# Kernel optimization log

Measured on AMD Instinct MI355X. Metric: run time of the kernel, lower is better.

Reference implementation:

```python
import jax, jax.numpy as jnp
import numpy as np
from jax import lax

B, R, L = 8, 40, 128
IN = 256           # in_size
WDIM = 2 * IN      # word_h feature dim
DREL = 15          # dep_rel_emb_size
F = 200            # num_filters
FH = FW = 3        # filter size
HID = 300          # filter_factory_hidden

leaky = lambda x: jax.nn.leaky_relu(x, 0.01)


def setup_inputs() -> dict:
    key = jax.random.key(0)
    ks = jax.random.split(key, 16)
    s = lambda fan_in: (2.0 / fan_in) ** 0.5  # kaiming-ish scale
    inp = {
        "energy": jax.random.uniform(ks[0], (B, R, L, L), jnp.float32),
        "word_h": jax.random.normal(ks[1], (B, L, WDIM), jnp.float32),
        "e1": jax.random.normal(ks[2], (B, WDIM), jnp.float32),
        "e2": jax.random.normal(ks[3], (B, WDIM), jnp.float32),
        "sent_len": jax.random.randint(ks[4], (B,), 1, L, jnp.int64 if jax.config.jax_enable_x64 else jnp.int32),
        # params
        "rel_embs": jax.random.normal(ks[5], (R, DREL), jnp.float32) * s(DREL),
        "arc_W": jax.random.normal(ks[6], (IN, 4 * IN + DREL), jnp.float32) * s(4 * IN + DREL),
        "arc_b": jnp.zeros((IN,), jnp.float32),
        "ff_W": jax.random.normal(ks[7], (HID, 4 * IN), jnp.float32) * s(4 * IN),
        "ff_b": jnp.zeros((HID,), jnp.float32),
        "fw1": jax.random.normal(ks[8], (F, IN, FH, FW, HID), jnp.float32) * s(HID),
        "fb1": jax.random.normal(ks[9], (F, IN, FH, FW), jnp.float32) * 0.02,
        "it_W": jax.random.normal(ks[10], (F, 4 * IN), jnp.float32) * s(4 * IN),
        "it_b": jnp.zeros((F,), jnp.float32),
    }
    return inp


def _forward(energy, word_h, e1, e2, rel_embs, arc_W, arc_b, ff_W, ff_b, fw1, fb1, it_W, it_b):
    # threshold mask (energy_threshold = 0.0)
    energy = jnp.where(energy < 0.0, 0.0, energy)

    # ---- get_arc_representations ----
    marginal = energy.sum(axis=1)                                  # [B,L,L]
    rel_tensor = jnp.einsum('brij,rd->bijd', energy, rel_embs)     # [B,L,L,DREL]
    # combine_two_tensors(word_h, word_h): Z[b,i,j] = [X[b,j], Y[b,i]]
    X2 = jnp.broadcast_to(word_h[:, None, :, :], (B, L, L, WDIM))
    Y2 = jnp.broadcast_to(word_h[:, :, None, :], (B, L, L, WDIM))
    dep_head = jnp.concatenate([X2, Y2], axis=-1) * marginal[..., None]  # [B,L,L,4*IN]
    all_t = jnp.concatenate([dep_head, rel_tensor], axis=-1)       # [B,L,L,4*IN+DREL]
    arc = leaky(jnp.einsum('bijk,ok->bijo', all_t, arc_W) + arc_b) # [B,L,L,IN]
    mem_bank = jnp.transpose(arc, (0, 3, 1, 2))                    # [B,IN,L,L]

    # ---- filter factory (dropout = identity at eval) ----
    inputs = jnp.concatenate([e1, e2], axis=-1)                    # [B,4*IN]
    h = leaky(inputs @ ff_W.T + ff_b)                              # [B,HID]
    filt = leaky(jnp.einsum('fdhwk,bk->bfdhw', fw1, h) + fb1)      # [B,F,IN,3,3]

    # ---- per-sample conv2d, batched via vmap ----
    def conv_one(x, w):  # x: [IN,L,L], w: [F,IN,3,3]
        return lax.conv_general_dilated(x[None], w, (1, 1), 'VALID',
                                        dimension_numbers=('NCHW', 'OIHW', 'NCHW'))[0]
    out = jax.vmap(conv_one)(mem_bank, filt)                       # [B,F,L-2,L-2]
    result = leaky(out).reshape(B, F, -1).max(axis=-1)             # adaptive max pool -> [B,F]

    transformed = leaky(inputs @ it_W.T + it_b)                    # [B,F]
    return transformed + result


def reference(energy, word_h, e1, e2, sent_len, rel_embs, arc_W, arc_b,
              ff_W, ff_b, fw1, fb1, it_W, it_b):
    del sent_len  # unused by the original forward path
    return _forward(energy, word_h, e1, e2, rel_embs, arc_W, arc_b,
                    ff_W, ff_b, fw1, fb1, it_W, it_b)
```

## Files before the change

kernel.cpp:

```cpp
#include <hip/hip_runtime.h>
#include <stdint.h>


#define LK(x) ((x) > 0.f ? (x) : 0.01f*(x))

typedef __attribute__((ext_vector_type(8))) short s16x8;
typedef __attribute__((ext_vector_type(4))) float f32x4;

__device__ __forceinline__ unsigned short f2bf(float f) {
  union { float f; unsigned int u; } v; v.f = f;
  unsigned int u = v.u;
  return (unsigned short)((u + 0x7FFFu + ((u >> 16) & 1u)) >> 16);
}

__device__ __forceinline__ void gload_lds16(const void* g, void* l) {
  __builtin_amdgcn_global_load_lds(
      (const __attribute__((address_space(1))) unsigned int*)g,
      (__attribute__((address_space(3))) unsigned int*)l, 16, 0, 0);
}

__global__ __launch_bounds__(256) void k_prep(
    const float* __restrict__ e1, const float* __restrict__ e2,
    const float* __restrict__ rel, const float* __restrict__ aW,
    const float* __restrict__ ffW, const float* __restrict__ ffb,
    const float* __restrict__ itW, const float* __restrict__ itb,
    const float* __restrict__ wh,
    unsigned short* __restrict__ whbf, unsigned short* __restrict__ aw1,
    unsigned short* __restrict__ aw2, unsigned short* __restrict__ rwt,
    float* __restrict__ hg, float* __restrict__ trans)
{
  int bid = blockIdx.x, t = threadIdx.x;
  if (bid < 16) {
    __shared__ float in_lds[1024];
    int b = bid & 7;
    for (int k = t; k < 1024; k += 256)
      in_lds[k] = (k < 512) ? e1[b*512 + k] : e2[b*512 + (k - 512)];
    __syncthreads();
    if (bid < 8) {
      for (int o = t; o < 300; o += 256) {
        const float4* wr = (const float4*)(ffW + (size_t)o*1024);
        float acc = ffb[o];
        for (int k = 0; k < 256; ++k) {
          float4 w = wr[k]; float4 v = *(const float4*)&in_lds[k*4];
          acc += w.x*v.x + w.y*v.y + w.z*v.z + w.w*v.w;
        }
        hg[b*300 + o] = LK(acc);
      }
    } else {
      for (int o = t; o < 200; o += 256) {
        const float4* wr = (const float4*)(itW + (size_t)o*1024);
        float acc = itb[o];
        for (int k = 0; k < 256; ++k) {
          float4 w = wr[k]; float4 v = *(const float4*)&in_lds[k*4];
          acc += w.x*v.x + w.y*v.y + w.z*v.z + w.w*v.w;
        }
        trans[b*200 + o] = LK(acc);
      }
    }
  } else if (bid < 80) {
    int id0 = (bid - 16)*256 + t;
    for (int v = id0; v < 131072; v += 64*256) {
      float4 x = ((const float4*)wh)[v];
      unsigned short* dst = whbf + (size_t)v*4;
      dst[0] = f2bf(x.x); dst[1] = f2bf(x.y); dst[2] = f2bf(x.z); dst[3] = f2bf(x.w);
    }
  } else if (bid < 144) {
    int id0 = (bid - 80)*256 + t;
    for (int e = id0; e < 131072; e += 64*256) {
      int o = e >> 9, k = e & 511;
      aw1[e] = f2bf(aW[(size_t)o*1039 + k]);
      aw2[e] = f2bf(aW[(size_t)o*1039 + 512 + k]);
    }
  } else {
    int o = t;
    for (int r = 0; r < 40; ++r) {
      float s = 0.f;
      for (int d = 0; d < 15; ++d) s += rel[r*15 + d] * aW[(size_t)o*1039 + 1024 + d];
      rwt[o*72 + r] = f2bf(s);
    }
    for (int r = 40; r < 72; ++r) rwt[o*72 + r] = 0;
  }
}

__global__ __launch_bounds__(256) void k_pq(
    const unsigned short* __restrict__ whbf,
    const unsigned short* __restrict__ aw1,
    const unsigned short* __restrict__ aw2,
    float* __restrict__ Pg, float* __restrict__ Qg)
{
  int bid = blockIdx.x, t = threadIdx.x;
  int g = bid >> 8;
  int wv = t >> 6, l = t & 63, lm = l & 15, hi = l >> 4;
  int tile = (bid & 255)*4 + wv;
  int ot = tile & 15, nt = tile >> 4;
  const unsigned short* A = g ? aw2 : aw1;
  float* out = g ? Qg : Pg;
  int orow = ot*16 + lm, n = nt*16 + lm;
  f32x4 acc = {0.f, 0.f, 0.f, 0.f};
  const unsigned short* ap = A + (size_t)orow*512 + hi*8;
  const unsigned short* bp = whbf + (size_t)n*512 + hi*8;
#pragma unroll
  for (int kk = 0; kk < 16; ++kk) {
    s16x8 af = *(const s16x8*)(ap + kk*32);
    s16x8 bf = *(const s16x8*)(bp + kk*32);
    acc = __builtin_amdgcn_mfma_f32_16x16x32_bf16(bf, af, acc, 0, 0, 0);
  }
  int nb = nt*16 + hi*4, o = ot*16 + lm;
#pragma unroll
  for (int r = 0; r < 4; ++r)
    out[(size_t)(nb + r)*256 + o] = acc[r];
}

__global__ __launch_bounds__(256) void k_filt(
    const float* __restrict__ fw1, const float* __restrict__ fb1,
    const float* __restrict__ hg, unsigned short* __restrict__ filtX)
{
  int bid = blockIdx.x, t = threadIdx.x;
  __shared__ __align__(16) unsigned short Abuf[64*320];
  __shared__ __align__(16) unsigned short Bbuf[16*320];
  int r0 = bid*64;
  for (int idx = t; idx < 640; idx += 256) {
    int n = idx / 40, kc = idx - (idx/40)*40;
    unsigned w[4];
#pragma unroll
    for (int j = 0; j < 8; j += 2) {
      int k = kc*8 + j;
      float a = (n < 8 && k   < 300) ? hg[n*300 + k]     : 0.f;
      float b = (n < 8 && k+1 < 300) ? hg[n*300 + k + 1] : 0.f;
      w[j>>1] = (unsigned)f2bf(a) | ((unsigned)f2bf(b) << 16);
    }
    int byte = (n*640 + kc*16) ^ ((n & 7) << 4);
    *(uint4*)((char*)Bbuf + byte) = *(uint4*)w;
  }
  const float4* src = (const float4*)(fw1 + (size_t)r0*300);
  for (int i = 0; i < 19; ++i) {
    int c4 = t + i*256;
    if (c4 < 4800) {
      float4 v = src[c4];
      int row = c4 / 75, k = (c4 - row*75)*4;
      unsigned lo  = (unsigned)f2bf(v.x) | ((unsigned)f2bf(v.y) << 16);
      unsigned hi2 = (unsigned)f2bf(v.z) | ((unsigned)f2bf(v.w) << 16);
      int byte = (row*640 + k*2) ^ ((row & 7) << 4);
      *(unsigned long long*)((char*)Abuf + byte) =
          (unsigned long long)lo | ((unsigned long long)hi2 << 32);
    }
  }
  for (int idx = t; idx < 320; idx += 256) {
    int row = idx / 5, c = idx - (idx/5)*5;
    int byte = (row*640 + 600 + c*8) ^ ((row & 7) << 4);
    *(unsigned long long*)((char*)Abuf + byte) = 0ULL;
  }
  __syncthreads();
  int wv = t >> 6, l = t & 63, lm = l & 15, hi = l >> 4;
  int arow = wv*16 + lm;
  f32x4 acc = {0.f, 0.f, 0.f, 0.f};
#pragma unroll
  for (int ks = 0; ks < 10; ++ks) {
    int abyte = (arow*640 + ks*64 + hi*16) ^ ((arow & 7) << 4);
    int bbyte = (lm*640   + ks*64 + hi*16) ^ ((lm   & 7) << 4);
    s16x8 af = *(const s16x8*)((char*)Abuf + abyte);
    s16x8 bf = *(const s16x8*)((char*)Bbuf + bbyte);
    acc = __builtin_amdgcn_mfma_f32_16x16x32_bf16(af, bf, acc, 0, 0, 0);
  }
  if (lm < 8) {
#pragma unroll
    for (int r = 0; r < 4; ++r) {
      int wrow = r0 + wv*16 + hi*4 + r;
      float v = LK(acc[r] + fb1[wrow]);
      filtX[(size_t)wrow*8 + lm] = f2bf(v);
    }
  }
}

__global__ __launch_bounds__(256) void k_tr(
    const unsigned short* __restrict__ filtX,
    unsigned short* __restrict__ filtg)
{
  __shared__ unsigned short sh[8*2312];
  int bid = blockIdx.x, t = threadIdx.x;
  int dc = bid >> 5, fch = bid & 31;
  if (fch >= 25) {
    uint4 z = {0,0,0,0};
#pragma unroll
    for (int i = 0; i < 9; ++i) {
      int idx = t + i*256;
      int b = idx / 288, rem = idx - b*288;
      char* dst = (char*)filtg + ((size_t)(b*8+dc)*256 + fch*8)*576 + rem*16;
      *(uint4*)dst = z;
    }
    return;
  }
#pragma unroll
  for (int i = 0; i < 9; ++i) {
    int rr = t + i*256;
    int f_loc = rr / 288, e = rr - f_loc*288;
    int dl = e / 9, tap = e - dl*9;
    size_t wrow = (size_t)(fch*8 + f_loc)*2304 + dc*288 + e;
    uint4 v = *(const uint4*)((const char*)filtX + wrow*16);
    const unsigned short* pv = (const unsigned short*)&v;
    int base = f_loc*288 + tap*32 + dl;
#pragma unroll
    for (int b = 0; b < 8; ++b)
      sh[b*2312 + base] = pv[b];
  }
  __syncthreads();
#pragma unroll
  for (int i = 0; i < 9; ++i) {
    int idx = t + i*256;
    int b = idx / 288, rem = idx - b*288;
    uint4 v = *(const uint4*)((const char*)sh + b*4624 + rem*16);
    char* dst = (char*)filtg + ((size_t)(b*8+dc)*256 + fch*8)*576 + rem*16;
    *(uint4*)dst = v;
  }
}

__global__ __launch_bounds__(256) void k_arc(
    const float* __restrict__ energy,
    const unsigned short* __restrict__ rwt,
    const float* __restrict__ Pg, const float* __restrict__ Qg,
    const float* __restrict__ arcb,
    unsigned short* __restrict__ memb)
{
  __shared__ unsigned short Et[128*72];
  __shared__ float mpart[256];
  __shared__ float qlds[256];
  __shared__ float blds[256];
  int bid = blockIdx.x, t = threadIdx.x;
  int b = bid >> 7, i = bid & 127;
  int jj = t & 127, half = t >> 7;
  float macc = 0.f;
  for (int rr = 0; rr < 20; ++rr) {
    int r = half*20 + rr;
    float e = energy[(((size_t)b*40 + r)*128 + i)*128 + jj];
    e = fmaxf(e, 0.f);
    macc += e;
    Et[jj*72 + r] = f2bf(e);
  }
  mpart[t] = macc;
  if (t < 128) {
#pragma unroll
    for (int r = 40; r < 72; ++r) Et[t*72 + r] = 0;
  }
  qlds[t] = Qg[((size_t)(b*128 + i))*256 + t];
  blds[t] = arcb[t];
  __syncthreads();

  int wv = t >> 6, l = t & 63, lm = l & 15, hi = l >> 4;
  unsigned short* mout = memb + ((size_t)(b*128 + i))*128*256;
  for (int otl = 0; otl < 4; ++otl) {
    int ocb = (wv*4 + otl)*16;
    const unsigned short* rp = rwt + (ocb + lm)*72 + hi*8;
    s16x8 rw0 = *(const s16x8*)rp;
    s16x8 rw1 = *(const s16x8*)(rp + 32);
    int oc0 = ocb + hi*4;
    float4 q4 = *(const float4*)&qlds[oc0];
    float4 b4 = *(const float4*)&blds[oc0];
    for (int jt = 0; jt < 8; ++jt) {
      const unsigned short* ep = &Et[(jt*16 + lm)*72 + hi*8];
      s16x8 et0 = *(const s16x8*)ep;
      s16x8 et1 = *(const s16x8*)(ep + 32);
      f32x4 acc = {0.f,0.f,0.f,0.f};
      acc = __builtin_amdgcn_mfma_f32_16x16x32_bf16(rw0, et0, acc, 0, 0, 0);
      acc = __builtin_amdgcn_mfma_f32_16x16x32_bf16(rw1, et1, acc, 0, 0, 0);
      int j = jt*16 + lm;
      float m = mpart[j] + mpart[128 + j];
      float4 p4 = *(const float4*)&Pg[((size_t)(b*128 + j))*256 + oc0];
      unsigned long long pk = 0;
#pragma unroll
      for (int r = 0; r < 4; ++r) {
        float pr = (r==0)?p4.x:((r==1)?p4.y:((r==2)?p4.z:p4.w));
        float qr = (r==0)?q4.x:((r==1)?q4.y:((r==2)?q4.z:q4.w));
        float br = (r==0)?b4.x:((r==1)?b4.y:((r==2)?b4.z:b4.w));
        float v = acc[r] + m*(pr + qr) + br;
        v = LK(v);
        pk |= ((unsigned long long)f2bf(v)) << (16*r);
      }
      *(unsigned long long*)(mout + (size_t)j*256 + oc0) = pk;
    }
  }
}

__global__ __launch_bounds__(256, 2) void k_conv(
    const unsigned short* __restrict__ filtg,
    const unsigned short* __restrict__ memb,
    float* __restrict__ part)
{
  __shared__ __align__(16) char smem[50688];
  int t = threadIdx.x;
  int bid = (blockIdx.x & 7)*128 + (blockIdx.x >> 3);
  int yq = bid & 31;
  int tmp = bid >> 5;
  int fc = tmp & 3, b = tmp >> 2;
  int y0 = yq*4;
  int wv = t >> 6, l = t & 63, lm = l & 15, hi = l >> 4;
  int wx = wv & 1, wf = wv >> 1;

  f32x4 zero = {0.f,0.f,0.f,0.f};
  f32x4 acc[4][4][2];
#pragma unroll
  for (int yb = 0; yb < 4; ++yb)
#pragma unroll
    for (int xt = 0; xt < 4; ++xt) { acc[yb][xt][0] = zero; acc[yb][xt][1] = zero; }

  const char* fb0 = (const char*)filtg +
      ((size_t)(b*8)*256 + fc*64 + wf*32 + lm)*576 + hi*16;

  for (int dc = 0; dc < 8; ++dc) {
    s16x8 freg[2][9];
    const char* fdc = fb0 + (size_t)dc*(256*576);
#pragma unroll
    for (int ft = 0; ft < 2; ++ft)
#pragma unroll
      for (int tap = 0; tap < 9; ++tap)
        freg[ft][tap] = *(const s16x8*)(fdc + ft*(16*576) + tap*64);
    for (int c = wv; c < 50; c += 4) {
      int id = c*64 + l;
      if (id < 3168) {
        int ky = id / 528;
        int rem = id - ky*528;
        int x = rem >> 2, s = rem & 3;
        int cs = s ^ ((x >> 1) & 3);
        int xs = (x < 128) ? x : 127;
        int row = y0 + ky; if (row > 127) row = 127;
        const char* ms = (const char*)memb +
            (((((size_t)(b*128 + row))*128 + xs)*256) + dc*32 + cs*8)*2;
        gload_lds16(ms, smem + c*1024);
      }
    }
    __syncthreads();
#pragma unroll
    for (int r = 0; r < 6; ++r) {
#pragma unroll
      for (int kx = 0; kx < 3; ++kx) {
#pragma unroll
        for (int xt = 0; xt < 4; ++xt) {
          int x = wx*64 + xt*16 + lm + kx;
          int slot = hi ^ ((x >> 1) & 3);
          s16x8 af = *(const s16x8*)(smem + ((r*132 + x)*4 + slot)*16);
#pragma unroll
          for (int yb = 0; yb < 4; ++yb) {
            const int ky = r - yb;
            if (ky >= 0 && ky <= 2) {
              acc[yb][xt][0] = __builtin_amdgcn_mfma_f32_16x16x32_bf16(af, freg[0][ky*3+kx], acc[yb][xt][0], 0,0,0);
              acc[yb][xt][1] = __builtin_amdgcn_mfma_f32_16x16x32_bf16(af, freg[1][ky*3+kx], acc[yb][xt][1], 0,0,0);
            }
          }
        }
      }
    }
    __syncthreads();
  }

  float pm[4][2];
#pragma unroll
  for (int yb = 0; yb < 4; ++yb) { pm[yb][0] = -3.4e38f; pm[yb][1] = -3.4e38f; }
#pragma unroll
  for (int yb = 0; yb < 4; ++yb)
#pragma unroll
    for (int xt = 0; xt < 4; ++xt) {
      int xb = wx*64 + xt*16 + hi*4;
#pragma unroll
      for (int r = 0; r < 4; ++r) {
        if (xb + r < 126) {
          pm[yb][0] = fmaxf(pm[yb][0], acc[yb][xt][0][r]);
          pm[yb][1] = fmaxf(pm[yb][1], acc[yb][xt][1][r]);
        }
      }
    }
#pragma unroll
  for (int yb = 0; yb < 4; ++yb)
#pragma unroll
    for (int ft = 0; ft < 2; ++ft) {
      pm[yb][ft] = fmaxf(pm[yb][ft], __shfl_xor(pm[yb][ft], 16));
      pm[yb][ft] = fmaxf(pm[yb][ft], __shfl_xor(pm[yb][ft], 32));
    }
  float* red = (float*)smem;
  if (l < 16) {
#pragma unroll
    for (int yb = 0; yb < 4; ++yb)
#pragma unroll
      for (int ft = 0; ft < 2; ++ft)
        red[(yb*4 + wf*2 + wx)*32 + ft*16 + lm] = pm[yb][ft];
  }
  __syncthreads();
  {
    int yb = t >> 6, tt = t & 63;
    int wfi = tt >> 5, fi = tt & 31;
    if (y0 + yb < 126) {
      float v = fmaxf(red[(yb*4 + wfi*2 + 0)*32 + fi], red[(yb*4 + wfi*2 + 1)*32 + fi]);
      v = LK(v);
      part[((size_t)(b*126 + y0 + yb))*256 + fc*64 + tt] = v;
    }
  }
}

__global__ __launch_bounds__(256) void k_final(
    const float* __restrict__ part, const float* __restrict__ trans,
    float* __restrict__ out)
{
  int bid = blockIdx.x, t = threadIdx.x;
  int b = bid >> 3, fg = bid & 7;
  int f = fg*32 + (t >> 3), ys = t & 7;
  float m = -3.4e38f;
  for (int yy = ys; yy < 126; yy += 8)
    m = fmaxf(m, part[((size_t)(b*126 + yy))*256 + f]);
  m = fmaxf(m, __shfl_xor(m, 1));
  m = fmaxf(m, __shfl_xor(m, 2));
  m = fmaxf(m, __shfl_xor(m, 4));
  if (ys == 0 && f < 200)
    out[b*200 + f] = trans[b*200 + f] + m;
}

extern "C" void kernel_launch(void* const* d_in, const int* in_sizes, int n_in,
                              void* d_out, int out_size, void* d_ws, size_t ws_size,
                              hipStream_t stream)
{
  (void)in_sizes; (void)n_in; (void)out_size; (void)ws_size;
  const float* energy = (const float*)d_in[0];
  const float* word_h = (const float*)d_in[1];
  const float* e1     = (const float*)d_in[2];
  const float* e2     = (const float*)d_in[3];
  const float* rel    = (const float*)d_in[5];
  const float* aW     = (const float*)d_in[6];
  const float* arcb   = (const float*)d_in[7];
  const float* ffW    = (const float*)d_in[8];
  const float* ffb    = (const float*)d_in[9];
  const float* fw1    = (const float*)d_in[10];
  const float* fb1    = (const float*)d_in[11];
  const float* itW    = (const float*)d_in[12];
  const float* itb    = (const float*)d_in[13];

  char* ws = (char*)d_ws;
  unsigned short* whbf  = (unsigned short*)(ws + 0);
  unsigned short* aw1   = (unsigned short*)(ws + 1048576);
  unsigned short* aw2   = (unsigned short*)(ws + 1310720);
  unsigned short* rwt   = (unsigned short*)(ws + 1572864);
  float*          hg    = (float*)(ws + 1609728);
  float*          trans = (float*)(ws + 1619328);
  float*          Pg    = (float*)(ws + 1625728);
  float*          Qg    = (float*)(ws + 2674304);
  float*          part  = (float*)(ws + 3722880);
  unsigned short* filtg = (unsigned short*)(ws + 4755072);
  unsigned short* memb  = (unsigned short*)(ws + 14454400);
  unsigned short* filtX = (unsigned short*)(ws + 81563264);

  k_prep <<<145, 256, 0, stream>>>(e1, e2, rel, aW, ffW, ffb, itW, itb, word_h,
                                   whbf, aw1, aw2, rwt, hg, trans);
  k_pq   <<<512, 256, 0, stream>>>(whbf, aw1, aw2, Pg, Qg);
  k_filt <<<7200, 256, 0, stream>>>(fw1, fb1, hg, filtX);
  k_tr   <<<256, 256, 0, stream>>>(filtX, filtg);
  k_arc  <<<1024, 256, 0, stream>>>(energy, rwt, Pg, Qg, arcb, memb);
  k_conv <<<1024, 256, 0, stream>>>(filtg, memb, part);
  k_final<<<64, 256, 0, stream>>>(part, trans, (float*)d_out);
}
```

Measured before the change: 366.3 us.

## Parallelize prep GEMVs across waves and stream fw1 directly into MFMA registers

The small e1/e2 matvecs in k_prep previously ran on 16 blocks with one thread per output looping over 1024 inputs. They now run on 1000 blocks, each wave computing one output with a 64-lane shuffle reduction. In k_filt the fw1 tile is no longer staged through swizzled LDS: each lane loads its fp32 row slice from global memory, converts it to bf16 in registers and feeds it straight to the MFMA. This drops a large LDS buffer and a staging pass, at the cost of less coalesced global reads in k_filt.

```diff
diff --git a/kernel.cpp b/kernel.cpp
--- a/kernel.cpp
+++ b/kernel.cpp
@@ -30,42 +30,40 @@
     float* __restrict__ hg, float* __restrict__ trans)
 {
   int bid = blockIdx.x, t = threadIdx.x;
-  if (bid < 16) {
-    __shared__ float in_lds[1024];
-    int b = bid & 7;
-    for (int k = t; k < 1024; k += 256)
-      in_lds[k] = (k < 512) ? e1[b*512 + k] : e2[b*512 + (k - 512)];
-    __syncthreads();
-    if (bid < 8) {
-      for (int o = t; o < 300; o += 256) {
-        const float4* wr = (const float4*)(ffW + (size_t)o*1024);
-        float acc = ffb[o];
-        for (int k = 0; k < 256; ++k) {
-          float4 w = wr[k]; float4 v = *(const float4*)&in_lds[k*4];
-          acc += w.x*v.x + w.y*v.y + w.z*v.z + w.w*v.w;
-        }
-        hg[b*300 + o] = LK(acc);
-      }
-    } else {
-      for (int o = t; o < 200; o += 256) {
-        const float4* wr = (const float4*)(itW + (size_t)o*1024);
-        float acc = itb[o];
-        for (int k = 0; k < 256; ++k) {
-          float4 w = wr[k]; float4 v = *(const float4*)&in_lds[k*4];
-          acc += w.x*v.x + w.y*v.y + w.z*v.z + w.w*v.w;
-        }
-        trans[b*200 + o] = LK(acc);
-      }
-    }
-  } else if (bid < 80) {
-    int id0 = (bid - 16)*256 + t;
+  if (bid < 1000) {
+    int wv = t >> 6, l = t & 63;
+    bool ish = bid < 600;
+    int idx = ish ? bid*4 + wv : (bid - 600)*4 + wv;
+    int ob = ish ? 300 : 200;
+    int b = idx / ob, o = idx - b*ob;
+    const float* W = ish ? ffW : itW;
+    const float* bias = ish ? ffb : itb;
+    const float4* wr = (const float4*)(W + (size_t)o*1024) + l*4;
+    const float* inb = (l < 32) ? (e1 + b*512 + l*16)
+                                : (e2 + b*512 + (l - 32)*16);
+    float s = 0.f;
+#pragma unroll
+    for (int q = 0; q < 4; ++q) {
+      float4 w = wr[q];
+      float4 v = *(const float4*)(inb + q*4);
+      s += w.x*v.x + w.y*v.y + w.z*v.z + w.w*v.w;
+    }
+#pragma unroll
+    for (int sh = 1; sh < 64; sh <<= 1)
+      s += __shfl_xor(s, sh);
+    if (l == 0) {
+      float r = LK(s + bias[o]);
+      if (ish) hg[b*300 + o] = r; else trans[b*200 + o] = r;
+    }
+  } else if (bid < 1064) {
+    int id0 = (bid - 1000)*256 + t;
     for (int v = id0; v < 131072; v += 64*256) {
       float4 x = ((const float4*)wh)[v];
       unsigned short* dst = whbf + (size_t)v*4;
       dst[0] = f2bf(x.x); dst[1] = f2bf(x.y); dst[2] = f2bf(x.z); dst[3] = f2bf(x.w);
     }
-  } else if (bid < 144) {
-    int id0 = (bid - 80)*256 + t;
+  } else if (bid < 1128) {
+    int id0 = (bid - 1064)*256 + t;
     for (int e = id0; e < 131072; e += 64*256) {
       int o = e >> 9, k = e & 511;
       aw1[e] = f2bf(aW[(size_t)o*1039 + k]);
@@ -115,9 +113,8 @@
     const float* __restrict__ fw1, const float* __restrict__ fb1,
     const float* __restrict__ hg, unsigned short* __restrict__ filtX)
 {
-  int bid = blockIdx.x, t = threadIdx.x;
-  __shared__ __align__(16) unsigned short Abuf[64*320];
   __shared__ __align__(16) unsigned short Bbuf[16*320];
+  int bid = blockIdx.x, t = threadIdx.x;
   int r0 = bid*64;
   for (int idx = t; idx < 640; idx += 256) {
     int n = idx / 40, kc = idx - (idx/40)*40;
@@ -132,33 +129,30 @@
     int byte = (n*640 + kc*16) ^ ((n & 7) << 4);
     *(uint4*)((char*)Bbuf + byte) = *(uint4*)w;
   }
-  const float4* src = (const float4*)(fw1 + (size_t)r0*300);
-  for (int i = 0; i < 19; ++i) {
-    int c4 = t + i*256;
-    if (c4 < 4800) {
-      float4 v = src[c4];
-      int row = c4 / 75, k = (c4 - row*75)*4;
-      unsigned lo  = (unsigned)f2bf(v.x) | ((unsigned)f2bf(v.y) << 16);
-      unsigned hi2 = (unsigned)f2bf(v.z) | ((unsigned)f2bf(v.w) << 16);
-      int byte = (row*640 + k*2) ^ ((row & 7) << 4);
-      *(unsigned long long*)((char*)Abuf + byte) =
-          (unsigned long long)lo | ((unsigned long long)hi2 << 32);
-    }
-  }
-  for (int idx = t; idx < 320; idx += 256) {
-    int row = idx / 5, c = idx - (idx/5)*5;
-    int byte = (row*640 + 600 + c*8) ^ ((row & 7) << 4);
-    *(unsigned long long*)((char*)Abuf + byte) = 0ULL;
-  }
   __syncthreads();
   int wv = t >> 6, l = t & 63, lm = l & 15, hi = l >> 4;
-  int arow = wv*16 + lm;
+  const float* arow_p = fw1 + (size_t)(r0 + wv*16 + lm)*300;
   f32x4 acc = {0.f, 0.f, 0.f, 0.f};
 #pragma unroll
   for (int ks = 0; ks < 10; ++ks) {
-    int abyte = (arow*640 + ks*64 + hi*16) ^ ((arow & 7) << 4);
-    int bbyte = (lm*640   + ks*64 + hi*16) ^ ((lm   & 7) << 4);
-    s16x8 af = *(const s16x8*)((char*)Abuf + abyte);
+    int k0 = ks*32 + hi*8;
+    float av[8];
+    if (k0 + 8 <= 300) {
+      float4 v0 = *(const float4*)(arow_p + k0);
+      float4 v1 = *(const float4*)(arow_p + k0 + 4);
+      av[0]=v0.x; av[1]=v0.y; av[2]=v0.z; av[3]=v0.w;
+      av[4]=v1.x; av[5]=v1.y; av[6]=v1.z; av[7]=v1.w;
+    } else {
+#pragma unroll
+      for (int e = 0; e < 8; ++e) {
+        int k = k0 + e;
+        av[e] = (k < 300) ? arow_p[k] : 0.f;
+      }
+    }
+    s16x8 af;
+#pragma unroll
+    for (int e = 0; e < 8; ++e) af[e] = (short)f2bf(av[e]);
+    int bbyte = (lm*640 + ks*64 + hi*16) ^ ((lm & 7) << 4);
     s16x8 bf = *(const s16x8*)((char*)Bbuf + bbyte);
     acc = __builtin_amdgcn_mfma_f32_16x16x32_bf16(af, bf, acc, 0, 0, 0);
   }
@@ -444,8 +438,8 @@
   unsigned short* memb  = (unsigned short*)(ws + 14454400);
   unsigned short* filtX = (unsigned short*)(ws + 81563264);
 
-  k_prep <<<145, 256, 0, stream>>>(e1, e2, rel, aW, ffW, ffb, itW, itb, word_h,
-                                   whbf, aw1, aw2, rwt, hg, trans);
+  k_prep <<<1129, 256, 0, stream>>>(e1, e2, rel, aW, ffW, ffb, itW, itb, word_h,
+                                    whbf, aw1, aw2, rwt, hg, trans);
   k_pq   <<<512, 256, 0, stream>>>(whbf, aw1, aw2, Pg, Qg);
   k_filt <<<7200, 256, 0, stream>>>(fw1, fb1, hg, filtX);
   k_tr   <<<256, 256, 0, stream>>>(filtX, filtg);
```

After: 328.8 us. -10.2%, faster.
